# Optimization experiments

Hardware: AMD Instinct MI355X
Metric: run time of the kernel (lower is better)

## Reference

```python
import jax, jax.numpy as jnp
import numpy as np

N_HEAD = 16
N_KV_HEAD = 4
HEAD_DIM = 128
RMS_EPS = 1.1920928955078125e-07  # torch float32 eps used by F.rms_norm default


def apply_rotary_emb(x, cos, sin):
    # x: [B,T,H,D]; cos/sin: [1,T,1,D/2]
    d = x.shape[-1] // 2
    x1, x2 = x[..., :d], x[..., d:]
    return jnp.concatenate([x1 * cos + x2 * sin, -x1 * sin + x2 * cos], axis=-1)


def rms_norm(x):
    return x * jax.lax.rsqrt(jnp.mean(x * x, axis=-1, keepdims=True) + RMS_EPS)


def setup_inputs() -> dict:
    key = jax.random.key(0)
    ks = jax.random.split(key, 7)
    B, T, C = 2, 2048, 2048
    return {
        "x": jax.random.normal(ks[0], (B, T, C), jnp.float32),
        "cos": jax.random.normal(ks[1], (1, T, 1, HEAD_DIM // 2), jnp.float32),
        "sin": jax.random.normal(ks[2], (1, T, 1, HEAD_DIM // 2), jnp.float32),
        "wq": jax.random.normal(ks[3], (C, N_HEAD * HEAD_DIM), jnp.float32) * 0.02,
        "wk": jax.random.normal(ks[4], (C, N_KV_HEAD * HEAD_DIM), jnp.float32) * 0.02,
        "wv": jax.random.normal(ks[5], (C, N_KV_HEAD * HEAD_DIM), jnp.float32) * 0.02,
        "wo": jax.random.normal(ks[6], (C, C), jnp.float32) * 0.02,
        "window_size": 512,
    }


def reference(x, cos, sin, wq, wk, wv, wo, window_size):
    B, T, C = x.shape
    H, KV, D = N_HEAD, N_KV_HEAD, HEAD_DIM
    rep = H // KV
    q = (x @ wq).reshape(B, T, H, D)
    k = (x @ wk).reshape(B, T, KV, D)
    v = (x @ wv).reshape(B, T, KV, D)
    q = rms_norm(apply_rotary_emb(q, cos, sin))
    k = rms_norm(apply_rotary_emb(k, cos, sin))
    # GQA: group query heads by kv head instead of materializing expanded K/V
    qg = q.reshape(B, T, KV, rep, D)
    scale = 1.0 / np.sqrt(D)
    scores = jnp.einsum('btkrd,bskd->bkrts', qg, k) * scale  # [B,KV,rep,T,S]
    row = jnp.arange(T)[:, None]
    col = jnp.arange(T)[None, :]
    mask = (col <= row) & (row - col <= window_size)  # causal & sliding window
    scores = jnp.where(mask, scores, jnp.finfo(scores.dtype).min)
    probs = jax.nn.softmax(scores, axis=-1)
    y = jnp.einsum('bkrts,bskd->btkrd', probs, v).reshape(B, T, H * D)
    return y @ wo
```

## Files before the change

### kernel.cpp

```cpp
#include <hip/hip_runtime.h>
#include <stdint.h>

typedef __attribute__((ext_vector_type(4))) float f32x4;
typedef __attribute__((ext_vector_type(8))) __bf16 bf16x8;
typedef __attribute__((ext_vector_type(4))) unsigned int u32x4;
typedef unsigned short u16;

#define B_DIM 2
#define T_DIM 2048
#define C_DIM 2048
#define H_Q   16
#define H_KV  4
#define HD    128
#define NQKV  3072
#define MTOK  4096
#define RMS_EPS 1.1920928955078125e-07f
#define Q_SCALE 0.12751749f

__device__ __forceinline__ u16 f2bf(float f) {
  union { float f; unsigned int u; } v; v.f = f;
  unsigned int r = v.u + 0x7FFFu + ((v.u >> 16) & 1u);
  return (u16)(r >> 16);
}
__device__ __forceinline__ float bf2f(u16 h) {
  union { unsigned int u; float f; } v; v.u = ((unsigned int)h) << 16;
  return v.f;
}
__device__ __forceinline__ f32x4 mfma16(bf16x8 a, bf16x8 b, f32x4 c) {
  return __builtin_amdgcn_mfma_f32_16x16x32_bf16(a, b, c, 0, 0, 0);
}
__device__ __forceinline__ void gl_lds16(const void* g, void* l) {
  __builtin_amdgcn_global_load_lds(
      (const __attribute__((address_space(1))) unsigned int*)g,
      (__attribute__((address_space(3))) unsigned int*)l, 16, 0, 0);
}

__global__ __launch_bounds__(256) void prep_kernel(const float* __restrict__ x,
                                                   const float* __restrict__ wq,
                                                   const float* __restrict__ wk,
                                                   const float* __restrict__ wv,
                                                   const float* __restrict__ wo,
                                                   u16* __restrict__ xb,
                                                   u16* __restrict__ wqkvb,
                                                   u16* __restrict__ wob) {
  __shared__ float tile[64][65];
  int bid = blockIdx.x, t = threadIdx.x;
  if (bid < 2560) {
    int nb = bid % 80, kb = bid / 80;
    const float* src; u16* dst; int srcN, nloc;
    if (nb < 32)      { src = wq; srcN = 2048; nloc = nb;      dst = wqkvb; }
    else if (nb < 40) { src = wk; srcN = 512;  nloc = nb - 32; dst = wqkvb + (size_t)2048 * 2048; }
    else if (nb < 48) { src = wv; srcN = 512;  nloc = nb - 40; dst = wqkvb + (size_t)2560 * 2048; }
    else              { src = wo; srcN = 2048; nloc = nb - 48; dst = wob; }
    int n0 = nloc * 64, k0 = kb * 64;
    #pragma unroll
    for (int idx = t; idx < 4096; idx += 256) {
      int r = idx >> 6, c = idx & 63;
      tile[r][c] = src[(size_t)(k0 + r) * srcN + n0 + c];
    }
    __syncthreads();
    #pragma unroll
    for (int idx = t; idx < 4096; idx += 256) {
      int r = idx >> 6, c = idx & 63;
      dst[(size_t)(n0 + r) * 2048 + k0 + c] = f2bf(tile[c][r]);
    }
  } else {
    int i = ((bid - 2560) * 256 + t) * 4;
    if (i >= MTOK * C_DIM) return;
    float4 v = *(const float4*)(x + i);
    u16 o0 = f2bf(v.x), o1 = f2bf(v.y), o2 = f2bf(v.z), o3 = f2bf(v.w);
    unsigned int lo = (unsigned int)o0 | ((unsigned int)o1 << 16);
    unsigned int hi = (unsigned int)o2 | ((unsigned int)o3 << 16);
    *(uint2*)(xb + i) = make_uint2(lo, hi);
  }
}

__global__ __launch_bounds__(256) void ropevt_kernel(u16* __restrict__ qkv,
                                                     const float* __restrict__ cosb,
                                                     const float* __restrict__ sinb,
                                                     u16* __restrict__ vt) {
  __shared__ __align__(16) u16 tile[64][136];
  int bid = blockIdx.x, tid = threadIdx.x;
  if (bid < 256) {
    int tt0 = (bid & 31) * 64;
    int kvh = (bid >> 5) & 3;
    int b   = bid >> 7;
    const u16* vp = qkv + ((size_t)b * T_DIM + tt0) * NQKV + C_DIM + H_KV * HD + kvh * HD;
    #pragma unroll
    for (int i = 0; i < 4; ++i) {
      int cid = tid + i * 256;
      int r = cid >> 4, c = cid & 15;
      u32x4 v = *(const u32x4*)(vp + (size_t)r * NQKV + c * 8);
      *(u32x4*)&tile[r][c * 8] = v;
    }
    __syncthreads();
    u16* op = vt + ((size_t)(b * H_KV + kvh) * HD) * T_DIM + tt0;
    #pragma unroll
    for (int i = 0; i < 4; ++i) {
      int cid = tid + i * 256;
      int d = cid >> 3, tc = cid & 7;
      u16 vals[8];
      #pragma unroll
      for (int j = 0; j < 8; ++j) vals[j] = tile[tc * 8 + j][d];
      u32x4 w;
      w.x = (unsigned int)vals[0] | ((unsigned int)vals[1] << 16);
      w.y = (unsigned int)vals[2] | ((unsigned int)vals[3] << 16);
      w.z = (unsigned int)vals[4] | ((unsigned int)vals[5] << 16);
      w.w = (unsigned int)vals[6] | ((unsigned int)vals[7] << 16);
      *(u32x4*)(op + (size_t)d * T_DIM + tc * 8) = w;
    }
  } else {
    int gw = ((bid - 256) * 256 + tid) >> 6;
    int lane = tid & 63;
    int hh = gw % (H_Q + H_KV);
    int tok = gw / (H_Q + H_KV);
    int t = tok & (T_DIM - 1);
    bool isq = (hh < H_Q);
    int base = isq ? hh * HD : (C_DIM + (hh - H_Q) * HD);
    u16* p = qkv + (size_t)tok * NQKV + base;
    float x1 = bf2f(p[lane]);
    float x2 = bf2f(p[lane + 64]);
    float c = cosb[t * 64 + lane];
    float s = sinb[t * 64 + lane];
    float o1 =  x1 * c + x2 * s;
    float o2 = -x1 * s + x2 * c;
    float ss = o1 * o1 + o2 * o2;
    #pragma unroll
    for (int off = 1; off < 64; off <<= 1) ss += __shfl_xor(ss, off);
    float r = rsqrtf(ss * (1.0f / 128.0f) + RMS_EPS);
    if (isq) r *= Q_SCALE;
    p[lane]      = f2bf(o1 * r);
    p[lane + 64] = f2bf(o2 * r);
  }
}

template<int BF16OUT>
__global__ __launch_bounds__(256) void gemm_bt_kernel(const u16* __restrict__ A,
                                                      const u16* __restrict__ Bt,
                                                      void* __restrict__ Cv,
                                                      int M, int N, int K) {
  __shared__ __align__(16) u16 Asm[128 * 64];
  __shared__ __align__(16) u16 Bsm[128 * 64];
  const int tid = threadIdx.x;
  const int lane = tid & 63;
  const int wid = tid >> 6;
  const int m0 = blockIdx.y * 128, n0 = blockIdx.x * 128;
  const int wm = (wid >> 1) * 64, wn = (wid & 1) * 64;
  const int l15 = lane & 15, l4 = lane >> 4;
  const int csrc = (lane & 7) ^ (lane >> 3);
  f32x4 acc[4][4] = {};

  for (int k0 = 0; k0 < K; k0 += 64) {
    __syncthreads();
    #pragma unroll
    for (int i = 0; i < 4; ++i) {
      int g = wid * 4 + i;
      int row = g * 8 + (lane >> 3);
      gl_lds16(A  + (size_t)(m0 + row) * K + k0 + csrc * 8, (char*)Asm + g * 1024);
      gl_lds16(Bt + (size_t)(n0 + row) * K + k0 + csrc * 8, (char*)Bsm + g * 1024);
    }
    __syncthreads();
    #pragma unroll
    for (int ks = 0; ks < 2; ++ks) {
      bf16x8 af[4], bfr[4];
      #pragma unroll
      for (int mf = 0; mf < 4; ++mf) {
        int r = wm + mf * 16 + l15;
        int bo = r * 128 + (((ks * 4 + l4) ^ (r & 7)) * 16);
        af[mf] = __builtin_bit_cast(bf16x8, *(const u32x4*)((const char*)Asm + bo));
      }
      #pragma unroll
      for (int nf = 0; nf < 4; ++nf) {
        int r = wn + nf * 16 + l15;
        int bo = r * 128 + (((ks * 4 + l4) ^ (r & 7)) * 16);
        bfr[nf] = __builtin_bit_cast(bf16x8, *(const u32x4*)((const char*)Bsm + bo));
      }
      #pragma unroll
      for (int mf = 0; mf < 4; ++mf)
        #pragma unroll
        for (int nf = 0; nf < 4; ++nf)
          acc[mf][nf] = mfma16(af[mf], bfr[nf], acc[mf][nf]);
    }
  }
  #pragma unroll
  for (int mf = 0; mf < 4; ++mf)
    #pragma unroll
    for (int nf = 0; nf < 4; ++nf)
      #pragma unroll
      for (int reg = 0; reg < 4; ++reg) {
        int row = m0 + wm + mf * 16 + l4 * 4 + reg;
        int col = n0 + wn + nf * 16 + l15;
        float v = acc[mf][nf][reg];
        if (BF16OUT) ((u16*)Cv)[(size_t)row * N + col] = f2bf(v);
        else         ((float*)Cv)[(size_t)row * N + col] = v;
      }
}

__global__ __launch_bounds__(256, 4) void attn_kernel(const u16* __restrict__ qkv,
                                                      const u16* __restrict__ vt,
                                                      u16* __restrict__ yb,
                                                      const int* __restrict__ wsz_p) {
  __shared__ __align__(16) u16 Ksm[2][64 * 128];
  __shared__ __align__(16) u16 Vsm[2][128 * 64];
  __shared__ __align__(16) u16 Psm[4 * 16 * 64];

  const int W = wsz_p[0];
  const int tid = threadIdx.x, lane = tid & 63, wid = tid >> 6;
  const int l15 = lane & 15, l4 = lane >> 4;
  const int bid = blockIdx.x;
  const int h   = bid & 15;
  const int b   = (bid >> 4) & 1;
  const int qt  = 31 - (bid >> 5);
  const int kvh = h >> 2;
  const size_t tokb = (size_t)b * T_DIM;
  const u16* vtb = vt + ((size_t)(b * H_KV + kvh) * HD) * T_DIM;
  const int rbase = qt * 64 + wid * 16;

  auto stage = [&](int kt, int bufsel) {
    const u16* kp = qkv + (tokb + kt * 64) * NQKV + C_DIM + kvh * HD;
    #pragma unroll
    for (int i = 0; i < 4; ++i) {
      int g = wid * 4 + i;
      int row = g * 4 + (lane >> 4);
      int cs = (lane & 15) ^ (row & 15);
      gl_lds16(kp + (size_t)row * NQKV + cs * 8, (char*)Ksm[bufsel] + g * 1024);
    }
    const u16* vp = vtb + kt * 64;
    #pragma unroll
    for (int i = 0; i < 4; ++i) {
      int g = wid * 4 + i;
      int d = g * 8 + (lane >> 3);
      int cs = (lane & 7) ^ (d & 7);
      gl_lds16(vp + (size_t)d * T_DIM + cs * 8, (char*)Vsm[bufsel] + g * 1024);
    }
  };

  bf16x8 qf[4];
  {
    int r = rbase + l15;
    const u16* qp = qkv + (tokb + r) * NQKV + h * HD;
    #pragma unroll
    for (int ks = 0; ks < 4; ++ks)
      qf[ks] = __builtin_bit_cast(bf16x8, *(const u32x4*)(qp + ks * 32 + l4 * 8));
  }

  const u32x4 onesu = {0x3F803F80u, 0x3F803F80u, 0x3F803F80u, 0x3F803F80u};
  const bf16x8 onesf = __builtin_bit_cast(bf16x8, onesu);

  f32x4 yacc[8] = {};
  f32x4 ylsum = {0.f, 0.f, 0.f, 0.f};
  float mrow[4];
  #pragma unroll
  for (int rg = 0; rg < 4; ++rg) mrow[rg] = -3.0e38f;

  int smin = qt * 64 - W; if (smin < 0) smin = 0;
  const int t0 = smin >> 6;
  char* pbase = (char*)Psm + wid * 2048;

  stage(t0, 0);
  __syncthreads();
  int cur = 0;

  for (int kt = t0; kt <= qt; ++kt) {
    if (kt < qt) stage(kt + 1, cur ^ 1);

    const int slo = kt * 64;
    bool active = (slo <= rbase + 15) && ((rbase - (slo + 63)) <= W);
    if (active) {
      float Sc[4][4];
      __builtin_amdgcn_s_setprio(1);
      #pragma unroll
      for (int nf = 0; nf < 4; ++nf) {
        f32x4 sa = {0.f, 0.f, 0.f, 0.f};
        int key = nf * 16 + l15;
        #pragma unroll
        for (int ks = 0; ks < 4; ++ks) {
          int bo = key * 256 + (((ks * 4 + l4) ^ (key & 15)) * 16);
          bf16x8 kf = __builtin_bit_cast(bf16x8, *(const u32x4*)((const char*)Ksm[cur] + bo));
          sa = mfma16(qf[ks], kf, sa);
        }
        #pragma unroll
        for (int rg = 0; rg < 4; ++rg) Sc[nf][rg] = sa[rg];
      }
      __builtin_amdgcn_s_setprio(0);
      bool fullvalid = ((slo + 63) <= rbase) && ((rbase + 15 - slo) <= W);
      if (!fullvalid) {
        #pragma unroll
        for (int nf = 0; nf < 4; ++nf) {
          int s = slo + nf * 16 + l15;
          #pragma unroll
          for (int rg = 0; rg < 4; ++rg) {
            int r = rbase + l4 * 4 + rg;
            if (s > r || (r - s) > W) Sc[nf][rg] = -3.0e38f;
          }
        }
      }
      float tmax[4];
      #pragma unroll
      for (int rg = 0; rg < 4; ++rg) {
        float tm = fmaxf(fmaxf(Sc[0][rg], Sc[1][rg]), fmaxf(Sc[2][rg], Sc[3][rg]));
        #pragma unroll
        for (int off = 1; off < 16; off <<= 1) tm = fmaxf(tm, __shfl_xor(tm, off));
        tmax[rg] = tm;
      }
      bool small = tmax[0] <= mrow[0] + 8.f && tmax[1] <= mrow[1] + 8.f &&
                   tmax[2] <= mrow[2] + 8.f && tmax[3] <= mrow[3] + 8.f;
      if (!__all(small)) {
        f32x4 fv;
        #pragma unroll
        for (int rg = 0; rg < 4; ++rg) {
          float mnew = fmaxf(mrow[rg], tmax[rg]);
          fv[rg] = exp2f(fmaxf(mrow[rg], -1.0e30f) - fmaxf(mnew, -1.0e30f));
          mrow[rg] = mnew;
        }
        #pragma unroll
        for (int nf2 = 0; nf2 < 8; ++nf2) yacc[nf2] *= fv;
        ylsum *= fv;
      }
      float mc[4];
      #pragma unroll
      for (int rg = 0; rg < 4; ++rg) mc[rg] = fmaxf(mrow[rg], -1.0e30f);
      #pragma unroll
      for (int nf = 0; nf < 4; ++nf)
        #pragma unroll
        for (int rg = 0; rg < 4; ++rg) {
          float pv = exp2f(Sc[nf][rg] - mc[rg]);
          unsigned int pbits = __builtin_bit_cast(unsigned int, pv);
          int q   = l4 * 4 + rg;
          int key = nf * 16 + l15;
          int bo = q * 128 + (((key >> 3) ^ (q & 7)) * 16) + (key & 7) * 2;
          *(u16*)(pbase + bo) = (u16)(pbits >> 16);
        }

      #pragma unroll
      for (int ks2 = 0; ks2 < 2; ++ks2) {
        int boA = l15 * 128 + (((ks2 * 4 + l4) ^ (l15 & 7)) * 16);
        bf16x8 pa = __builtin_bit_cast(bf16x8, *(const u32x4*)(pbase + boA));
        __builtin_amdgcn_s_setprio(1);
        ylsum = mfma16(pa, onesf, ylsum);
        #pragma unroll
        for (int nf2 = 0; nf2 < 8; ++nf2) {
          int d = nf2 * 16 + l15;
          int boB = d * 128 + (((ks2 * 4 + l4) ^ (d & 7)) * 16);
          bf16x8 vf = __builtin_bit_cast(bf16x8, *(const u32x4*)((const char*)Vsm[cur] + boB));
          yacc[nf2] = mfma16(pa, vf, yacc[nf2]);
        }
        __builtin_amdgcn_s_setprio(0);
      }
    }
    __syncthreads();
    cur ^= 1;
  }

  #pragma unroll
  for (int nf2 = 0; nf2 < 8; ++nf2)
    #pragma unroll
    for (int rg = 0; rg < 4; ++rg) {
      int r = rbase + l4 * 4 + rg;
      float v = yacc[nf2][rg] / ylsum[rg];
      yb[(tokb + r) * (size_t)C_DIM + h * HD + nf2 * 16 + l15] = f2bf(v);
    }
}

extern "C" void kernel_launch(void* const* d_in, const int* in_sizes, int n_in,
                              void* d_out, int out_size, void* d_ws, size_t ws_size,
                              hipStream_t stream) {
  const float* x    = (const float*)d_in[0];
  const float* cosb = (const float*)d_in[1];
  const float* sinb = (const float*)d_in[2];
  const float* wq   = (const float*)d_in[3];
  const float* wk   = (const float*)d_in[4];
  const float* wv   = (const float*)d_in[5];
  const float* wo   = (const float*)d_in[6];
  const int*   wsz  = (const int*)d_in[7];

  char* ws = (char*)d_ws;
  u16* xb    = (u16*)(ws);
  u16* qkvb  = (u16*)(ws + (size_t)16777216);
  u16* wqkvb = (u16*)(ws + (size_t)41943040);
  u16* wob   = (u16*)(ws + (size_t)54525952);
  u16* ybuf  = (u16*)(ws + (size_t)62914560);
  u16* vtb   = (u16*)(ws);

  prep_kernel<<<2560 + 8192, 256, 0, stream>>>(x, wq, wk, wv, wo, xb, wqkvb, wob);
  gemm_bt_kernel<1><<<dim3(NQKV / 128, MTOK / 128), 256, 0, stream>>>(xb, wqkvb, qkvb, MTOK, NQKV, C_DIM);
  ropevt_kernel<<<256 + (MTOK * (H_Q + H_KV)) / 4, 256, 0, stream>>>(qkvb, cosb, sinb, vtb);
  attn_kernel<<<B_DIM * H_Q * (T_DIM / 64), 256, 0, stream>>>(qkvb, vtb, ybuf, wsz);
  gemm_bt_kernel<0><<<dim3(C_DIM / 128, MTOK / 128), 256, 0, stream>>>(ybuf, wob, d_out, MTOK, C_DIM, C_DIM);
}
```

Measured before the change: 187.3 us.

## Compute transposed scores and move P into A-operand via lane shuffles instead of LDS

Swaps the MFMA operands so each lane holds scores for one query row across keys, making the row max a per-lane reduction with only two cross-lane shuffles. The softmax probabilities are packed to bf16 pairs in registers and redistributed into the PV A-operand layout with __shfl, replacing the per-wave LDS round trip through Psm. This removes LDS store/load traffic and frees shared memory, at the cost of many ds_bpermute shuffles and selects, plus extra shuffles to broadcast rescale factors.

```diff
diff --git a/kernel.cpp b/kernel.cpp
--- a/kernel.cpp
+++ b/kernel.cpp
@@ -202,7 +202,6 @@
                                                       const int* __restrict__ wsz_p) {
   __shared__ __align__(16) u16 Ksm[2][64 * 128];
   __shared__ __align__(16) u16 Vsm[2][128 * 64];
-  __shared__ __align__(16) u16 Psm[4 * 16 * 64];
 
   const int W = wsz_p[0];
   const int tid = threadIdx.x, lane = tid & 63, wid = tid >> 6;
@@ -249,13 +248,13 @@
 
   f32x4 yacc[8] = {};
   f32x4 ylsum = {0.f, 0.f, 0.f, 0.f};
-  float mrow[4];
-  #pragma unroll
-  for (int rg = 0; rg < 4; ++rg) mrow[rg] = -3.0e38f;
+  float mq = -3.0e38f;
 
   int smin = qt * 64 - W; if (smin < 0) smin = 0;
   const int t0 = smin >> 6;
-  char* pbase = (char*)Psm + wid * 2048;
+  const int idxA = l15 + ((l4 & 1) << 5);
+  const int idxB = idxA + 16;
+  const bool hiNf = ((l4 >> 1) & 1) != 0;
 
   stage(t0, 0);
   __syncthreads();
@@ -277,7 +276,7 @@
         for (int ks = 0; ks < 4; ++ks) {
           int bo = key * 256 + (((ks * 4 + l4) ^ (key & 15)) * 16);
           bf16x8 kf = __builtin_bit_cast(bf16x8, *(const u32x4*)((const char*)Ksm[cur] + bo));
-          sa = mfma16(qf[ks], kf, sa);
+          sa = mfma16(kf, qf[ks], sa);
         }
         #pragma unroll
         for (int rg = 0; rg < 4; ++rg) Sc[nf][rg] = sa[rg];
@@ -285,57 +284,61 @@
       __builtin_amdgcn_s_setprio(0);
       bool fullvalid = ((slo + 63) <= rbase) && ((rbase + 15 - slo) <= W);
       if (!fullvalid) {
-        #pragma unroll
-        for (int nf = 0; nf < 4; ++nf) {
-          int s = slo + nf * 16 + l15;
+        int q = rbase + l15;
+        #pragma unroll
+        for (int nf = 0; nf < 4; ++nf)
           #pragma unroll
           for (int rg = 0; rg < 4; ++rg) {
-            int r = rbase + l4 * 4 + rg;
-            if (s > r || (r - s) > W) Sc[nf][rg] = -3.0e38f;
+            int s = slo + nf * 16 + l4 * 4 + rg;
+            if (s > q || (q - s) > W) Sc[nf][rg] = -3.0e38f;
           }
-        }
-      }
-      float tmax[4];
-      #pragma unroll
-      for (int rg = 0; rg < 4; ++rg) {
-        float tm = fmaxf(fmaxf(Sc[0][rg], Sc[1][rg]), fmaxf(Sc[2][rg], Sc[3][rg]));
-        #pragma unroll
-        for (int off = 1; off < 16; off <<= 1) tm = fmaxf(tm, __shfl_xor(tm, off));
-        tmax[rg] = tm;
-      }
-      bool small = tmax[0] <= mrow[0] + 8.f && tmax[1] <= mrow[1] + 8.f &&
-                   tmax[2] <= mrow[2] + 8.f && tmax[3] <= mrow[3] + 8.f;
-      if (!__all(small)) {
+      }
+      float tm = Sc[0][0];
+      #pragma unroll
+      for (int nf = 0; nf < 4; ++nf)
+        #pragma unroll
+        for (int rg = 0; rg < 4; ++rg) tm = fmaxf(tm, Sc[nf][rg]);
+      tm = fmaxf(tm, __shfl_xor(tm, 16));
+      tm = fmaxf(tm, __shfl_xor(tm, 32));
+      if (!__all(tm <= mq + 8.f)) {
+        float mnew = fmaxf(mq, tm);
+        float fq = exp2f(fmaxf(mq, -1.0e30f) - fmaxf(mnew, -1.0e30f));
+        mq = mnew;
         f32x4 fv;
         #pragma unroll
         for (int rg = 0; rg < 4; ++rg) {
-          float mnew = fmaxf(mrow[rg], tmax[rg]);
-          fv[rg] = exp2f(fmaxf(mrow[rg], -1.0e30f) - fmaxf(mnew, -1.0e30f));
-          mrow[rg] = mnew;
+          int ql = l4 * 4 + rg;
+          fv[rg] = __shfl(fq, (lane & 0x30) | ql);
         }
         #pragma unroll
         for (int nf2 = 0; nf2 < 8; ++nf2) yacc[nf2] *= fv;
         ylsum *= fv;
       }
-      float mc[4];
-      #pragma unroll
-      for (int rg = 0; rg < 4; ++rg) mc[rg] = fmaxf(mrow[rg], -1.0e30f);
-      #pragma unroll
-      for (int nf = 0; nf < 4; ++nf)
-        #pragma unroll
-        for (int rg = 0; rg < 4; ++rg) {
-          float pv = exp2f(Sc[nf][rg] - mc[rg]);
-          unsigned int pbits = __builtin_bit_cast(unsigned int, pv);
-          int q   = l4 * 4 + rg;
-          int key = nf * 16 + l15;
-          int bo = q * 128 + (((key >> 3) ^ (q & 7)) * 16) + (key & 7) * 2;
-          *(u16*)(pbase + bo) = (u16)(pbits >> 16);
-        }
+      float mqc = fmaxf(mq, -1.0e30f);
+      unsigned int P32[4][2];
+      #pragma unroll
+      for (int nf = 0; nf < 4; ++nf) {
+        unsigned int b0 = __builtin_bit_cast(unsigned int, exp2f(Sc[nf][0] - mqc));
+        unsigned int b1 = __builtin_bit_cast(unsigned int, exp2f(Sc[nf][1] - mqc));
+        unsigned int b2 = __builtin_bit_cast(unsigned int, exp2f(Sc[nf][2] - mqc));
+        unsigned int b3 = __builtin_bit_cast(unsigned int, exp2f(Sc[nf][3] - mqc));
+        P32[nf][0] = (b1 & 0xFFFF0000u) | (b0 >> 16);
+        P32[nf][1] = (b3 & 0xFFFF0000u) | (b2 >> 16);
+      }
 
       #pragma unroll
       for (int ks2 = 0; ks2 < 2; ++ks2) {
-        int boA = l15 * 128 + (((ks2 * 4 + l4) ^ (l15 & 7)) * 16);
-        bf16x8 pa = __builtin_bit_cast(bf16x8, *(const u32x4*)(pbase + boA));
+        int nf0 = 2 * ks2, nf1 = 2 * ks2 + 1;
+        unsigned int a00 = __shfl(P32[nf0][0], idxA), a10 = __shfl(P32[nf1][0], idxA);
+        unsigned int a01 = __shfl(P32[nf0][1], idxA), a11 = __shfl(P32[nf1][1], idxA);
+        unsigned int b00 = __shfl(P32[nf0][0], idxB), b10 = __shfl(P32[nf1][0], idxB);
+        unsigned int b01 = __shfl(P32[nf0][1], idxB), b11 = __shfl(P32[nf1][1], idxB);
+        u32x4 paw;
+        paw.x = hiNf ? a10 : a00;
+        paw.y = hiNf ? a11 : a01;
+        paw.z = hiNf ? b10 : b00;
+        paw.w = hiNf ? b11 : b01;
+        bf16x8 pa = __builtin_bit_cast(bf16x8, paw);
         __builtin_amdgcn_s_setprio(1);
         ylsum = mfma16(pa, onesf, ylsum);
         #pragma unroll
```

Result: no change. 185.1 us, median of 2 (-1.2%).
